# Optimization experiments

Measured on AMD Instinct MI355X. Metric: run time of the kernel, lower is better.

The kernel has to match this reference:

```python
import jax, jax.numpy as jnp
import numpy as np

B, L, D = 8, 8192, 128
NC, N, H = 8, 64, 16          # chunks, d_state, chunk_size
NLAYERS, COND, RED = 3, 32, 64
OUT_DIMS = (1, 1, 100, 192, 64, 12, 5)  # f0,A,amps,hmag,nmag,formants(4*3),expression


def _ln(x, g, b, eps=1e-5):
    m = jnp.mean(x, -1, keepdims=True)
    v = jnp.mean((x - m) ** 2, -1, keepdims=True)
    return (x - m) / jnp.sqrt(v + eps) * g + b


def _s4_block(x, g, b, inW, inb, outW, outb, lre, lim, Bn, Cre, Cim, Dc):
    # ParallelS4Layer: LN -> in_proj -> per-chunk S4 FFT conv (fused/batched) -> out_proj -> SiLU -> residual
    Bt, Lt, Dt = x.shape
    z = _ln(x, g, b) @ inW + inb
    u = z.reshape(Bt, Lt, NC, H)
    t = jnp.arange(Lt, dtype=jnp.float32)
    E = jnp.exp((lre + 1j * lim)[:, :, None] * t)                       # [NC,N,L] Vandermonde
    k = jnp.real(jnp.einsum('cn,cnl->cl', (Cre + 1j * Cim) * Bn, E))    # [NC,L]
    k = jnp.concatenate([k, k[:, ::-1]], axis=-1)                        # bidirectional -> [NC,2L]
    kf = jnp.fft.rfft(k, n=2 * Lt, axis=-1)                              # [NC,L+1]
    uf = jnp.fft.rfft(u, n=2 * Lt, axis=1)                               # [B,L+1,NC,H]
    y = jnp.fft.irfft(uf * kf.T[None, :, :, None], n=2 * Lt, axis=1)[:, :Lt]
    y = (y + u * Dc[None, None, :, None]).reshape(Bt, Lt, Dt)           # skip term D
    return x + jax.nn.silu(y @ outW + outb)


def _forward(f0, phone_emb, singer_emb, lang_emb, inW, inb, inln_g, inln_b,
             s4_ln_g, s4_ln_b, s4_inW, s4_inb, s4_outW, s4_outb,
             lam_re, lam_im, Bn, C_re, C_im, Dc,
             attn_g, attn_lnb, attn_w, attn_bias, gpW, gpb,
             genW_s, genb_s, genW_sh, genb_sh, genW_h, genb_h, genW_o, genb_o,
             phone_seq, singer_id, language_id):
    Bt, Lt = phone_seq.shape
    pe = phone_emb[phone_seq]                                            # [B,L,64]
    se = jnp.broadcast_to(singer_emb[singer_id][:, None, :], (Bt, Lt, singer_emb.shape[1]))
    le = jnp.broadcast_to(lang_emb[language_id][:, None, :], (Bt, Lt, lang_emb.shape[1]))
    x = jnp.concatenate([pe, se, le, f0], axis=-1)                       # [B,L,113]
    h = jax.nn.silu(_ln(x @ inW + inb, inln_g, inln_b))                  # input_proj
    for i in range(NLAYERS):
        h = _s4_block(h, s4_ln_g[i], s4_ln_b[i], s4_inW[i], s4_inb[i],
                      s4_outW[i], s4_outb[i], lam_re[i], lam_im[i],
                      Bn[i], C_re[i], C_im[i], Dc[i])
    logits = _ln(h, attn_g, attn_lnb) @ attn_w + attn_bias[0]            # [B,L]
    a = jax.nn.softmax(logits, axis=1)
    g = jnp.einsum('bl,bld->bd', a, h) @ gpW + gpb                       # global cond [B,32]
    outs = []
    for i, d in enumerate(OUT_DIMS):
        scale = (g @ genW_s[i] + genb_s[i])[:, None, :]
        shift = (g @ genW_sh[i] + genb_sh[i])[:, None, :]
        r = jax.nn.silu((h * scale + shift) @ genW_h[i] + genb_h[i])
        outs.append(r @ genW_o[i, :, :d] + genb_o[i, :d])
    return jnp.concatenate(outs, axis=-1)                                # [B,L,375]


def setup_inputs() -> dict:
    ks = iter(jax.random.split(jax.random.key(0), 64))
    nk = lambda: next(ks)
    w = lambda *s: jax.random.normal(nk(), s, jnp.float32) * 0.02
    CIN = 64 + 32 + 16 + 1
    return {
        'phone_seq': jax.random.randint(nk(), (B, L), 0, 100),
        'singer_id': jax.random.randint(nk(), (B,), 0, 50),
        'language_id': jax.random.randint(nk(), (B,), 0, 10),
        'f0': jax.random.uniform(nk(), (B, L, 1), jnp.float32),
        'phone_emb': w(100, 64), 'singer_emb': w(50, 32), 'lang_emb': w(10, 16),
        'inW': w(CIN, D), 'inb': jnp.zeros((D,), jnp.float32),
        'inln_g': jnp.ones((D,), jnp.float32), 'inln_b': jnp.zeros((D,), jnp.float32),
        's4_ln_g': jnp.ones((NLAYERS, D), jnp.float32), 's4_ln_b': jnp.zeros((NLAYERS, D), jnp.float32),
        's4_inW': w(NLAYERS, D, D), 's4_inb': jnp.zeros((NLAYERS, D), jnp.float32),
        's4_outW': w(NLAYERS, D, D), 's4_outb': jnp.zeros((NLAYERS, D), jnp.float32),
        'lam_re': -0.5 * jnp.ones((NLAYERS, NC, N), jnp.float32),
        'lam_im': jnp.broadcast_to(jnp.arange(N, dtype=jnp.float32) * (2.0 * np.pi / N), (NLAYERS, NC, N)),
        'Bn': jax.random.normal(nk(), (NLAYERS, NC, N), jnp.float32),
        'C_re': jax.random.normal(nk(), (NLAYERS, NC, N), jnp.float32),
        'C_im': jax.random.normal(nk(), (NLAYERS, NC, N), jnp.float32),
        'Dc': jax.random.normal(nk(), (NLAYERS, NC), jnp.float32),
        'attn_g': jnp.ones((D,), jnp.float32), 'attn_lnb': jnp.zeros((D,), jnp.float32),
        'attn_w': w(D), 'attn_bias': jnp.zeros((1,), jnp.float32),
        'gpW': w(D, COND), 'gpb': jnp.zeros((COND,), jnp.float32),
        'genW_s': w(7, COND, D), 'genb_s': jnp.zeros((7, D), jnp.float32),
        'genW_sh': w(7, COND, D), 'genb_sh': jnp.zeros((7, D), jnp.float32),
        'genW_h': w(7, D, RED), 'genb_h': jnp.zeros((7, RED), jnp.float32),
        'genW_o': w(7, RED, 192), 'genb_o': jnp.zeros((7, 192), jnp.float32),
    }


def reference(phone_seq, singer_id, language_id, f0, phone_emb, singer_emb, lang_emb,
              inW, inb, inln_g, inln_b, s4_ln_g, s4_ln_b, s4_inW, s4_inb, s4_outW, s4_outb,
              lam_re, lam_im, Bn, C_re, C_im, Dc, attn_g, attn_lnb, attn_w, attn_bias,
              gpW, gpb, genW_s, genb_s, genW_sh, genb_sh, genW_h, genb_h, genW_o, genb_o):
    return _forward(f0, phone_emb, singer_emb, lang_emb, inW, inb, inln_g, inln_b,
                    s4_ln_g, s4_ln_b, s4_inW, s4_inb, s4_outW, s4_outb,
                    lam_re, lam_im, Bn, C_re, C_im, Dc,
                    attn_g, attn_lnb, attn_w, attn_bias, gpW, gpb,
                    genW_s, genb_s, genW_sh, genb_sh, genW_h, genb_h, genW_o, genb_o,
                    phone_seq, singer_id, language_id)
```

## Files before the change

### kernel.cpp

```cpp
#include <hip/hip_runtime.h>
#include <math.h>

#define BB 8
#define LL 8192
#define DD 128
#define NCH 8
#define NST 64
#define TAPS 32
#define NOUTD 375
#define NSEG 64

typedef __attribute__((ext_vector_type(8))) short bf16x8;
typedef __attribute__((ext_vector_type(4))) float f32x4;
#define MFMA16(a,b,c) __builtin_amdgcn_mfma_f32_16x16x32_bf16((a),(b),(c),0,0,0)

struct __align__(8) us4 { unsigned short x,y,z,w; };

__device__ __forceinline__ unsigned short f2b(float f) {
  unsigned x = __float_as_uint(f);
  unsigned r = (x + 0x7fffu + ((x >> 16) & 1u)) >> 16;
  return (unsigned short)r;
}
__device__ __forceinline__ float b2f(unsigned short u) {
  return __uint_as_float(((unsigned)u) << 16);
}
__device__ __forceinline__ float silu_f(float x){ return x / (1.f + expf(-x)); }

static constexpr size_t WS_H      = 0;
static constexpr size_t WS_LOGITS = WS_H      + (size_t)BB*LL*DD;
static constexpr size_t WS_SEGM   = WS_LOGITS + (size_t)BB*LL;
static constexpr size_t WS_SEGS   = WS_SEGM   + BB*NSEG;
static constexpr size_t WS_SEGV   = WS_SEGS   + BB*NSEG;
static constexpr size_t WS_SCALE  = WS_SEGV   + (size_t)BB*NSEG*DD;
static constexpr size_t WS_SHIFT  = WS_SCALE  + (size_t)7*BB*DD;
static constexpr size_t WS_C1     = WS_SHIFT  + (size_t)7*BB*DD;
static constexpr size_t WS_C2     = WS_C1     + 3*DD;
static constexpr size_t WS_KTAB   = WS_C2     + 3*DD;
static constexpr size_t WS_GAW    = WS_KTAB   + 3*NCH*TAPS;
static constexpr size_t WS_ASCAL  = WS_GAW    + DD;
static constexpr size_t WS_BASE   = WS_ASCAL  + 32;
static constexpr size_t WS_BIAS1  = WS_BASE   + BB*DD;
static constexpr size_t WS_ZB_F   = WS_BIAS1  + (size_t)BB*448;
static constexpr size_t WS_WGT_F  = WS_ZB_F   + (size_t)BB*LL*DD/2;
static constexpr size_t WS_WOT_F  = WS_WGT_F  + (size_t)3*DD*DD/2;
static constexpr size_t WS_WO2T_F = WS_WOT_F  + (size_t)3*DD*DD/2;
static constexpr size_t WS_WCT_F  = WS_WO2T_F + (size_t)7*192*64/2;
static constexpr size_t WS_TOTAL  = WS_WCT_F  + (size_t)BB*448*DD/2;

__device__ __constant__ int c_offs_d[7] = {0, 1, 2, 102, 294, 358, 370};
__device__ __constant__ int c_dims_d[7] = {1, 1, 100, 192, 64, 12, 5};
__device__ __constant__ int t_hd[27] = {0,1,2,2,2,2,2,2,2,3,3,3,3,3,3,3,3,3,3,3,3,4,4,4,4,5,6};
__device__ __constant__ int t_nl[27] = {0,0,0,1,2,3,4,5,6,0,1,2,3,4,5,6,7,8,9,10,11,0,1,2,3,0,0};

__global__ __launch_bounds__(256) void k0_setup(
    const float* s4_ln_g, const float* s4_ln_b, const float* s4_inW, const float* s4_inb,
    const float* s4_outW,
    const float* lam_re, const float* lam_im, const float* Bn, const float* Cre, const float* Cim,
    const float* attn_g, const float* attn_lnb, const float* attn_w, const float* attn_bias,
    const int* singer_id, const int* language_id,
    const float* singer_emb, const float* lang_emb, const float* inW, const float* inb,
    const float* genW_o, float* ws)
{
  int blk = blockIdx.x, tid = threadIdx.x;
  if (blk < 3) {
    __shared__ __align__(16) unsigned short tile[128*136];
    __shared__ float c1p[256], c2p[256];
    int ly = blk;
    int n = tid & 127;
    float c1a = 0.f, c2a = 0.f;
    for (int j = 0; j < 64; ++j) {
      int k = (tid >> 7) + 2*j;
      float v  = s4_inW[((size_t)ly*DD + k)*DD + n];
      float gk = s4_ln_g[ly*DD + k];
      float bk = s4_ln_b[ly*DD + k];
      tile[k*136 + n] = f2b(gk*v);
      c1a += gk*v; c2a += bk*v;
    }
    c1p[tid] = c1a; c2p[tid] = c2a;
    __syncthreads();
    if (tid < DD) {
      ws[WS_C1 + ly*DD + tid] = c1p[tid] + c1p[tid+128];
      ws[WS_C2 + ly*DD + tid] = c2p[tid] + c2p[tid+128] + s4_inb[ly*DD + tid];
    }
    unsigned short* wgt = (unsigned short*)(ws + WS_WGT_F);
    for (int o = tid; o < DD*DD; o += 256) {
      int nn = o >> 7, k = o & 127;
      wgt[ly*DD*DD + o] = tile[k*136 + nn];
    }
    __syncthreads();
    for (int j = 0; j < 64; ++j) {
      int k = (tid >> 7) + 2*j;
      tile[k*136 + n] = f2b(s4_outW[((size_t)ly*DD + k)*DD + n]);
    }
    __syncthreads();
    unsigned short* wot = (unsigned short*)(ws + WS_WOT_F);
    for (int o = tid; o < DD*DD; o += 256) {
      int nn = o >> 7, k = o & 127;
      wot[ly*DD*DD + o] = tile[k*136 + nn];
    }
  } else if (blk < 27) {
    __shared__ float part[256];
    int ly = (blk - 3) >> 3, cx = (blk - 3) & 7;
    int dt = tid & 31, nc = tid >> 5;
    const float* lre = lam_re + (ly*NCH + cx)*NST;
    const float* lim = lam_im + (ly*NCH + cx)*NST;
    const float* bn  = Bn  + (ly*NCH + cx)*NST;
    const float* cre = Cre + (ly*NCH + cx)*NST;
    const float* cim = Cim + (ly*NCH + cx)*NST;
    float td = (float)dt, acc = 0.f;
    for (int nn = nc*8; nn < nc*8 + 8; ++nn) {
      float e = expf(lre[nn]*td);
      float ang = lim[nn]*td;
      acc += bn[nn]*(cre[nn]*cosf(ang) - cim[nn]*sinf(ang))*e;
    }
    part[tid] = acc;
    __syncthreads();
    if (tid < 32) {
      float a = 0.f;
      #pragma unroll
      for (int i = 0; i < 8; ++i) a += part[i*32 + tid];
      ws[WS_KTAB + (ly*NCH + cx)*TAPS + tid] = a;
    }
  } else if (blk == 27) {
    for (int o = tid; o < BB*DD; o += 256) {
      int b = o >> 7, d = o & 127;
      int sid = singer_id[b], lid = language_id[b];
      float acc = inb[d];
      for (int j = 0; j < 32; ++j) acc += singer_emb[sid*32 + j]*inW[(64 + j)*DD + d];
      for (int j = 0; j < 16; ++j) acc += lang_emb[lid*16 + j]*inW[(96 + j)*DD + d];
      ws[WS_BASE + o] = acc;
    }
    if (tid < DD) ws[WS_GAW + tid] = attn_g[tid]*attn_w[tid];
    if (tid == 0) {
      float c1s = 0.f, c2s = 0.f;
      for (int d = 0; d < DD; ++d) { c1s += attn_g[d]*attn_w[d]; c2s += attn_lnb[d]*attn_w[d]; }
      ws[WS_ASCAL+0] = c1s;
      ws[WS_ASCAL+1] = c2s + attn_bias[0];
    }
  } else {
    __shared__ float gw[64*200];
    int hd = blk - 28;
    for (int k = 0; k < 64; ++k) {
      if (tid < 192) gw[k*200 + tid] = genW_o[((size_t)hd*64 + k)*192 + tid];
    }
    __syncthreads();
    unsigned short* wo2t = (unsigned short*)(ws + WS_WO2T_F);
    for (int o = tid; o < 192*64; o += 256) {
      int nn = o >> 6, k = o & 63;
      wo2t[(size_t)hd*192*64 + o] = f2b(gw[k*200 + nn]);
    }
  }
}

__global__ __launch_bounds__(256) void k1p_input(
    const int* phone_seq, const float* f0, const float* phone_emb,
    const float* inW, const float* inln_g, const float* inln_b, float* ws)
{
  __shared__ __align__(16) float pm[64*72];
  __shared__ __align__(16) unsigned short hm[64*136];
  __shared__ int   ps[64];
  __shared__ float fv[64];
  __shared__ float rs_s[64], mrs_s[64];
  int tid = threadIdx.x;
  size_t gbase = (size_t)blockIdx.x * 64;
  if (tid < 64) { ps[tid] = phone_seq[gbase + tid]; fv[tid] = f0[gbase + tid]; }
  __syncthreads();
  #pragma unroll
  for (int j = 0; j < 4; ++j) {
    int idx4 = tid + 256*j;
    int tok = idx4 >> 4, col = idx4 & 15;
    float4 v = *(const float4*)(phone_emb + (size_t)ps[tok]*64 + col*4);
    *(float4*)(pm + tok*72 + col*4) = v;
  }
  __syncthreads();
  int ti = tid >> 5, di = tid & 31, d0 = di*4;
  float acc[8][4];
  #pragma unroll
  for (int i = 0; i < 8; ++i) { acc[i][0]=0.f; acc[i][1]=0.f; acc[i][2]=0.f; acc[i][3]=0.f; }
  for (int kk = 0; kk < 64; kk += 4) {
    float4 w0 = *(const float4*)(inW + (kk+0)*DD + d0);
    float4 w1 = *(const float4*)(inW + (kk+1)*DD + d0);
    float4 w2 = *(const float4*)(inW + (kk+2)*DD + d0);
    float4 w3 = *(const float4*)(inW + (kk+3)*DD + d0);
    #pragma unroll
    for (int i = 0; i < 8; ++i) {
      float4 a = *(float4*)(pm + (ti*8 + i)*72 + kk);
      acc[i][0] += a.x*w0.x + a.y*w1.x + a.z*w2.x + a.w*w3.x;
      acc[i][1] += a.x*w0.y + a.y*w1.y + a.z*w2.y + a.w*w3.y;
      acc[i][2] += a.x*w0.z + a.y*w1.z + a.z*w2.z + a.w*w3.z;
      acc[i][3] += a.x*w0.w + a.y*w1.w + a.z*w2.w + a.w*w3.w;
    }
  }
  float4 w112 = *(const float4*)(inW + 112*DD + d0);
  int b = (int)(gbase >> 13);
  float4 bs  = *(const float4*)(ws + WS_BASE + b*DD + d0);
  float4 lg4 = *(const float4*)(inln_g + d0);
  float4 lb4 = *(const float4*)(inln_b + d0);
  float s2[8], ss2[8];
  #pragma unroll
  for (int i = 0; i < 8; ++i) {
    int tok = ti*8 + i;
    float fz = fv[tok];
    float y0 = acc[i][0] + fz*w112.x + bs.x;
    float y1 = acc[i][1] + fz*w112.y + bs.y;
    float y2 = acc[i][2] + fz*w112.z + bs.z;
    float y3 = acc[i][3] + fz*w112.w + bs.w;
    float s  = y0+y1+y2+y3;
    float ss = y0*y0+y1*y1+y2*y2+y3*y3;
    #pragma unroll
    for (int m = 16; m >= 1; m >>= 1) { s += __shfl_xor(s, m); ss += __shfl_xor(ss, m); }
    float mean = s * 0.0078125f;
    float var  = ss * 0.0078125f - mean*mean;
    float rstd = rsqrtf(var + 1e-5f);
    y0 = silu_f((y0 - mean)*rstd*lg4.x + lb4.x);
    y1 = silu_f((y1 - mean)*rstd*lg4.y + lb4.y);
    y2 = silu_f((y2 - mean)*rstd*lg4.z + lb4.z);
    y3 = silu_f((y3 - mean)*rstd*lg4.w + lb4.w);
    *(float4*)(ws + WS_H + (gbase + tok)*DD + d0) = make_float4(y0,y1,y2,y3);
    us4 p; p.x = f2b(y0); p.y = f2b(y1); p.z = f2b(y2); p.w = f2b(y3);
    *(us4*)(hm + tok*136 + d0) = p;
    s2[i]  = y0+y1+y2+y3;
    ss2[i] = y0*y0+y1*y1+y2*y2+y3*y3;
  }
  #pragma unroll
  for (int m = 16; m >= 1; m >>= 1) {
    #pragma unroll
    for (int i = 0; i < 8; ++i) { s2[i] += __shfl_xor(s2[i], m); ss2[i] += __shfl_xor(ss2[i], m); }
  }
  if (di == 0) {
    #pragma unroll
    for (int i = 0; i < 8; ++i) {
      int tok = ti*8 + i;
      float mean = s2[i]*0.0078125f;
      float var  = ss2[i]*0.0078125f - mean*mean;
      float rstd = rsqrtf(var + 1e-5f);
      rs_s[tok] = rstd; mrs_s[tok] = mean*rstd;
    }
  }
  __syncthreads();
  int w = tid >> 6, lane = tid & 63, q = lane >> 4, c = lane & 15;
  int m16 = w*16;
  const unsigned short* wgt = (const unsigned short*)(ws + WS_WGT_F);
  bf16x8 aF[4];
  #pragma unroll
  for (int kk = 0; kk < 4; ++kk)
    aF[kk] = *(const bf16x8*)(hm + (m16 + c)*136 + kk*32 + q*8);
  float rsv[4], mrv[4];
  #pragma unroll
  for (int r = 0; r < 4; ++r) { int row = m16 + q*4 + r; rsv[r] = rs_s[row]; mrv[r] = mrs_s[row]; }
  unsigned short* zb = (unsigned short*)(ws + WS_ZB_F);
  #pragma unroll
  for (int nt = 0; nt < 8; ++nt) {
    f32x4 za = {0.f,0.f,0.f,0.f};
    #pragma unroll
    for (int kk = 0; kk < 4; ++kk) {
      bf16x8 bF = *(const bf16x8*)(wgt + (nt*16 + c)*DD + kk*32 + q*8);
      za = MFMA16(aF[kk], bF, za);
    }
    int col = nt*16 + c;
    float c1v = ws[WS_C1 + col];
    float c2v = ws[WS_C2 + col];
    #pragma unroll
    for (int r = 0; r < 4; ++r) {
      float zv = rsv[r]*za[r] - mrv[r]*c1v + c2v;
      zb[(gbase + m16 + q*4 + r)*DD + col] = f2b(zv);
    }
  }
}

__global__ __launch_bounds__(256) void k3p_conv_out(
    float* ws, const float* s4_outb, const float* Dc, int ly, int do_logits, int do_z)
{
  __shared__ __align__(16) unsigned short zw[128*128];
  __shared__ __align__(16) unsigned short ym[64*136];
  __shared__ float k2t[8*64];
  __shared__ float dcs[8];
  __shared__ float rs2[64], mrs2[64];
  int tid = threadIdx.x, blk = blockIdx.x;
  int b  = blk >> 7;
  int t0 = (blk & 127) * 64;
  const unsigned short* zbp = (const unsigned short*)(ws + WS_ZB_F);
  #pragma unroll
  for (int j = 0; j < 8; ++j) {
    int idx8 = tid + 256*j;
    int tok = idx8 >> 4, c8 = idx8 & 15;
    int t = t0 - 32 + tok;
    bf16x8 v = {0,0,0,0,0,0,0,0};
    if (t >= 0 && t < LL) v = *(const bf16x8*)(zbp + ((size_t)b*LL + t)*DD + c8*8);
    *(bf16x8*)(zw + tok*DD + c8*8) = v;
  }
  for (int o = tid; o < 512; o += 256) {
    int c = o >> 6, m = o & 63;
    int idx = (m <= 31) ? (31 - m) : (m - 32);
    k2t[o] = ws[WS_KTAB + (ly*NCH + c)*TAPS + idx];
  }
  if (tid < 8) dcs[tid] = Dc[ly*NCH + tid];
  __syncthreads();
  #pragma unroll
  for (int p = 0; p < 2; ++p) {
    int half = p*2 + (tid >> 7), ch = tid & 127, cx = ch >> 4;
    int base = 1 + half*16;
    float ring[16], accv[16];
    #pragma unroll
    for (int x = 0; x < 16; ++x) { ring[x] = b2f(zw[(base + x)*DD + ch]); accv[x] = 0.f; }
    #pragma unroll
    for (int m = 0; m < 64; ++m) {
      float kf = k2t[cx*64 + m];
      #pragma unroll
      for (int i = 0; i < 16; ++i) accv[i] += kf * ring[(m + i) & 15];
      if (m < 63) ring[m & 15] = b2f(zw[(base + m + 16)*DD + ch]);
    }
    float dcv = dcs[cx];
    #pragma unroll
    for (int i = 0; i < 16; ++i) {
      int tl = half*16 + i;
      ym[tl*136 + ch] = f2b(accv[i] + dcv * b2f(zw[(32 + tl)*DD + ch]));
    }
  }
  __syncthreads();
  unsigned short* hm2 = zw;
  int w = tid >> 6, lane = tid & 63, q = lane >> 4, c = lane & 15;
  int m16 = w*16;
  const unsigned short* wot = (const unsigned short*)(ws + WS_WOT_F) + ly*DD*DD;
  bf16x8 aF[4];
  #pragma unroll
  for (int kk = 0; kk < 4; ++kk)
    aF[kk] = *(const bf16x8*)(ym + (m16 + c)*136 + kk*32 + q*8);
  float* hbuf = ws + WS_H;
  float c1s = ws[WS_ASCAL+0], c2s = ws[WS_ASCAL+1];
  float sr[4] = {0,0,0,0}, ssr[4] = {0,0,0,0}, dtr[4] = {0,0,0,0};
  #pragma unroll
  for (int nt = 0; nt < 8; ++nt) {
    f32x4 acc = {0.f,0.f,0.f,0.f};
    #pragma unroll
    for (int kk = 0; kk < 4; ++kk) {
      bf16x8 bF = *(const bf16x8*)(wot + (nt*16 + c)*DD + kk*32 + q*8);
      acc = MFMA16(aF[kk], bF, acc);
    }
    int col = nt*16 + c;
    float ob = s4_outb[ly*DD + col];
    float gw = ws[WS_GAW + col];
    #pragma unroll
    for (int r = 0; r < 4; ++r) {
      size_t gofs = ((size_t)b*LL + t0 + m16 + q*4 + r)*DD + col;
      float hold = hbuf[gofs];
      float hn = hold + silu_f(acc[r] + ob);
      hbuf[gofs] = hn;
      hm2[(m16 + q*4 + r)*136 + col] = f2b(hn);
      sr[r] += hn; ssr[r] += hn*hn;
      if (do_logits) dtr[r] += hn*gw;
    }
  }
  #pragma unroll
  for (int m = 8; m >= 1; m >>= 1) {
    #pragma unroll
    for (int r = 0; r < 4; ++r) {
      sr[r]  += __shfl_xor(sr[r],  m);
      ssr[r] += __shfl_xor(ssr[r], m);
      if (do_logits) dtr[r] += __shfl_xor(dtr[r], m);
    }
  }
  if (c < 4) {
    int r = c;
    float mean = sr[r]*0.0078125f;
    float var  = ssr[r]*0.0078125f - mean*mean;
    float rstd = rsqrtf(var + 1e-5f);
    int row = m16 + q*4 + r;
    if (do_z) { rs2[row] = rstd; mrs2[row] = mean*rstd; }
    if (do_logits)
      ws[WS_LOGITS + (size_t)b*LL + t0 + row] = rstd*dtr[r] - mean*rstd*c1s + c2s;
  }
  if (do_z) {
    __syncthreads();
    const unsigned short* wgt2 = (const unsigned short*)(ws + WS_WGT_F) + (ly+1)*DD*DD;
    bf16x8 aF2[4];
    #pragma unroll
    for (int kk = 0; kk < 4; ++kk)
      aF2[kk] = *(const bf16x8*)(hm2 + (m16 + c)*136 + kk*32 + q*8);
    float rsv[4], mrv[4];
    #pragma unroll
    for (int r = 0; r < 4; ++r) { int row = m16 + q*4 + r; rsv[r] = rs2[row]; mrv[r] = mrs2[row]; }
    unsigned short* zb = (unsigned short*)(ws + WS_ZB_F);
    size_t gbase = (size_t)b*LL + t0;
    #pragma unroll
    for (int nt = 0; nt < 8; ++nt) {
      f32x4 za = {0.f,0.f,0.f,0.f};
      #pragma unroll
      for (int kk = 0; kk < 4; ++kk) {
        bf16x8 bF = *(const bf16x8*)(wgt2 + (nt*16 + c)*DD + kk*32 + q*8);
        za = MFMA16(aF2[kk], bF, za);
      }
      int col = nt*16 + c;
      float c1v = ws[WS_C1 + (ly+1)*DD + col];
      float c2v = ws[WS_C2 + (ly+1)*DD + col];
      #pragma unroll
      for (int r = 0; r < 4; ++r) {
        float zv = rsv[r]*za[r] - mrv[r]*c1v + c2v;
        zb[(gbase + m16 + q*4 + r)*DD + col] = f2b(zv);
      }
    }
  }
}

__global__ __launch_bounds__(256) void k5b_pool(float* ws)
{
  int blk = blockIdx.x, tid = threadIdx.x;
  int b = blk >> 6, seg = blk & 63;
  const float* lg = ws + WS_LOGITS + (size_t)b*LL + seg*128;
  __shared__ float ev[128];
  __shared__ float red[4], red2[4];
  __shared__ float vr[2][128];
  float a0 = (tid < 128) ? lg[tid] : -1e30f;
  float mx = a0;
  #pragma unroll
  for (int m = 32; m >= 1; m >>= 1) mx = fmaxf(mx, __shfl_xor(mx, m));
  if ((tid & 63) == 0) red[tid >> 6] = mx;
  __syncthreads();
  float M = fmaxf(fmaxf(red[0], red[1]), fmaxf(red[2], red[3]));
  float e0 = (tid < 128) ? expf(a0 - M) : 0.f;
  if (tid < 128) ev[tid] = e0;
  float s = e0;
  #pragma unroll
  for (int m = 32; m >= 1; m >>= 1) s += __shfl_xor(s, m);
  if ((tid & 63) == 0) red2[tid >> 6] = s;
  __syncthreads();
  float S = red2[0] + red2[1] + red2[2] + red2[3];
  int ls = tid >> 7, d = tid & 127;
  const float* hb = ws + WS_H + ((size_t)b*LL + seg*128)*DD;
  float acc = 0.f;
  for (int jj = 0; jj < 64; ++jj) {
    int tok = jj*2 + ls;
    acc += ev[tok] * hb[(size_t)tok*DD + d];
  }
  vr[ls][d] = acc;
  __syncthreads();
  if (tid < 128) ws[WS_SEGV + (size_t)(b*NSEG + seg)*DD + tid] = vr[0][tid] + vr[1][tid];
  if (tid == 0) { ws[WS_SEGM + b*NSEG + seg] = M; ws[WS_SEGS + b*NSEG + seg] = S; }
}

__global__ __launch_bounds__(256) void k5c_cond(
    float* ws, const float* gpW, const float* gpb,
    const float* genW_s, const float* genb_s, const float* genW_sh, const float* genb_sh)
{
  __shared__ float wsg[NSEG];
  __shared__ float Ssh[1];
  __shared__ float gpre[DD];
  __shared__ float red[256];
  __shared__ float gg[32];
  int b = blockIdx.x, tid = threadIdx.x;
  if (tid == 0) {
    float M = -1e30f;
    for (int sg = 0; sg < NSEG; ++sg) M = fmaxf(M, ws[WS_SEGM + b*NSEG + sg]);
    float S = 0.f;
    for (int sg = 0; sg < NSEG; ++sg) {
      float e = expf(ws[WS_SEGM + b*NSEG + sg] - M);
      wsg[sg] = e;
      S += ws[WS_SEGS + b*NSEG + sg]*e;
    }
    Ssh[0] = S;
  }
  __syncthreads();
  if (tid < DD) {
    float V = 0.f;
    for (int sg = 0; sg < NSEG; ++sg)
      V += ws[WS_SEGV + (size_t)(b*NSEG + sg)*DD + tid]*wsg[sg];
    gpre[tid] = V / Ssh[0];
  }
  __syncthreads();
  {
    int c = tid & 31, kc = tid >> 5;
    float p = 0.f;
    for (int k = kc*16; k < kc*16 + 16; ++k) p += gpre[k]*gpW[k*32 + c];
    red[tid] = p;
  }
  __syncthreads();
  if (tid < 32) {
    float a = gpb[tid];
    #pragma unroll
    for (int i = 0; i < 8; ++i) a += red[i*32 + tid];
    gg[tid] = a;
  }
  __syncthreads();
  for (int o = tid; o < 7*DD; o += 256) {
    int hd = o >> 7, d = o & 127;
    float sc = genb_s[hd*DD + d], sh = genb_sh[hd*DD + d];
    for (int c = 0; c < 32; ++c) {
      float g = gg[c];
      sc += g*genW_s[((size_t)hd*32 + c)*DD + d];
      sh += g*genW_sh[((size_t)hd*32 + c)*DD + d];
    }
    ws[WS_SCALE + (size_t)hd*BB*DD + b*DD + d] = sc;
    ws[WS_SHIFT + (size_t)hd*BB*DD + b*DD + d] = sh;
  }
}

__global__ __launch_bounds__(256) void k5d_fold(float* ws, const float* genW_h, const float* genb_h)
{
  __shared__ float wh[128*65];
  __shared__ float red[256];
  int hd = blockIdx.x, tid = threadIdx.x;
  for (int o = tid; o < DD*64; o += 256) {
    int k = o >> 6, j = o & 63;
    wh[k*65 + j] = genW_h[(size_t)hd*DD*64 + o];
  }
  __syncthreads();
  unsigned short* wct = (unsigned short*)(ws + WS_WCT_F);
  for (int b = 0; b < BB; ++b) {
    const float* sc = ws + WS_SCALE + (size_t)hd*BB*DD + b*DD;
    const float* sh = ws + WS_SHIFT + (size_t)hd*BB*DD + b*DD;
    for (int o = tid; o < 64*DD; o += 256) {
      int j = o >> 7, k = o & 127;
      wct[((size_t)b*448 + hd*64 + j)*DD + k] = f2b(sc[k]*wh[k*65 + j]);
    }
    {
      int j = tid >> 2, kc = tid & 3;
      float p = 0.f;
      for (int k = kc*32; k < kc*32 + 32; ++k) p += sh[k]*wh[k*65 + j];
      red[tid] = p;
      __syncthreads();
      if (tid < 64)
        ws[WS_BIAS1 + b*448 + hd*64 + tid] =
          genb_h[hd*64 + tid] + red[tid*4] + red[tid*4+1] + red[tid*4+2] + red[tid*4+3];
      __syncthreads();
    }
  }
}

__global__ __launch_bounds__(512) void k6_heads(float* ws, const float* genb_o, float* out, int blk0)
{
  __shared__ __align__(16) unsigned short hm[64*136];
  __shared__ __align__(16) unsigned short rm[64*456];
  int tid = threadIdx.x, blk = blockIdx.x + blk0;
  int b = blk >> 7, t0 = (blk & 127)*64;
  const float* hb = ws + WS_H + ((size_t)b*LL + t0)*DD;
  #pragma unroll
  for (int j = 0; j < 4; ++j) {
    int idx4 = tid + 512*j;
    int tok = idx4 >> 5, c4 = idx4 & 31;
    float4 v = *(const float4*)(hb + (size_t)idx4*4);
    us4 p; p.x = f2b(v.x); p.y = f2b(v.y); p.z = f2b(v.z); p.w = f2b(v.w);
    *(us4*)(hm + tok*136 + c4*4) = p;
  }
  __syncthreads();
  int w = tid >> 6, lane = tid & 63, q = lane >> 4, c = lane & 15;
  int mi = w & 3, nh = w >> 2;
  int m16 = mi*16;
  {
    bf16x8 aF[4];
    #pragma unroll
    for (int kk = 0; kk < 4; ++kk)
      aF[kk] = *(const bf16x8*)(hm + (m16 + c)*136 + kk*32 + q*8);
    const unsigned short* wct = (const unsigned short*)(ws + WS_WCT_F) + (size_t)b*448*DD;
    #pragma unroll 2
    for (int ntl = 0; ntl < 14; ++ntl) {
      int nt = nh*14 + ntl;
      f32x4 acc = {0.f,0.f,0.f,0.f};
      #pragma unroll
      for (int kk = 0; kk < 4; ++kk) {
        bf16x8 bF = *(const bf16x8*)(wct + ((size_t)nt*16 + c)*DD + kk*32 + q*8);
        acc = MFMA16(aF[kk], bF, acc);
      }
      int col = nt*16 + c;
      float bias = ws[WS_BIAS1 + b*448 + col];
      #pragma unroll
      for (int r = 0; r < 4; ++r)
        rm[(m16 + q*4 + r)*456 + col] = f2b(silu_f(acc[r] + bias));
    }
  }
  __syncthreads();
  {
    const unsigned short* wo2t = (const unsigned short*)(ws + WS_WO2T_F);
    int i0 = (nh == 0) ? 0 : 14;
    int i1 = (nh == 0) ? 14 : 27;
    #pragma unroll 2
    for (int i = i0; i < i1; ++i) {
      int hd = t_hd[i], nl = t_nl[i];
      bf16x8 aF0 = *(const bf16x8*)(rm + (m16 + c)*456 + hd*64 + q*8);
      bf16x8 aF1 = *(const bf16x8*)(rm + (m16 + c)*456 + hd*64 + 32 + q*8);
      f32x4 acc = {0.f,0.f,0.f,0.f};
      bf16x8 bF0 = *(const bf16x8*)(wo2t + ((size_t)hd*192 + nl*16 + c)*64 + q*8);
      bf16x8 bF1 = *(const bf16x8*)(wo2t + ((size_t)hd*192 + nl*16 + c)*64 + 32 + q*8);
      acc = MFMA16(aF0, bF0, acc);
      acc = MFMA16(aF1, bF1, acc);
      int cl = nl*16 + c;
      int di = c_dims_d[hd];
      if (cl < di) {
        float bo = genb_o[hd*192 + cl];
        #pragma unroll
        for (int r = 0; r < 4; ++r)
          out[((size_t)b*LL + t0 + m16 + q*4 + r)*NOUTD + c_offs_d[hd] + cl] = acc[r] + bo;
      }
    }
  }
}

extern "C" void kernel_launch(void* const* d_in, const int* in_sizes, int n_in,
                              void* d_out, int out_size, void* d_ws, size_t ws_size,
                              hipStream_t stream) {
  const int*   phone_seq   = (const int*)  d_in[0];
  const int*   singer_id   = (const int*)  d_in[1];
  const int*   language_id = (const int*)  d_in[2];
  const float* f0          = (const float*)d_in[3];
  const float* phone_emb   = (const float*)d_in[4];
  const float* singer_emb  = (const float*)d_in[5];
  const float* lang_emb    = (const float*)d_in[6];
  const float* inW         = (const float*)d_in[7];
  const float* inb         = (const float*)d_in[8];
  const float* inln_g      = (const float*)d_in[9];
  const float* inln_b      = (const float*)d_in[10];
  const float* s4_ln_g     = (const float*)d_in[11];
  const float* s4_ln_b     = (const float*)d_in[12];
  const float* s4_inW      = (const float*)d_in[13];
  const float* s4_inb      = (const float*)d_in[14];
  const float* s4_outW     = (const float*)d_in[15];
  const float* s4_outb     = (const float*)d_in[16];
  const float* lam_re      = (const float*)d_in[17];
  const float* lam_im      = (const float*)d_in[18];
  const float* Bn          = (const float*)d_in[19];
  const float* C_re        = (const float*)d_in[20];
  const float* C_im        = (const float*)d_in[21];
  const float* Dc          = (const float*)d_in[22];
  const float* attn_g      = (const float*)d_in[23];
  const float* attn_lnb    = (const float*)d_in[24];
  const float* attn_w      = (const float*)d_in[25];
  const float* attn_bias   = (const float*)d_in[26];
  const float* gpW         = (const float*)d_in[27];
  const float* gpb         = (const float*)d_in[28];
  const float* genW_s      = (const float*)d_in[29];
  const float* genb_s      = (const float*)d_in[30];
  const float* genW_sh     = (const float*)d_in[31];
  const float* genb_sh     = (const float*)d_in[32];
  const float* genW_h      = (const float*)d_in[33];
  const float* genb_h      = (const float*)d_in[34];
  const float* genW_o      = (const float*)d_in[35];
  const float* genb_o      = (const float*)d_in[36];
  float* ws  = (float*)d_ws;
  float* out = (float*)d_out;

  k0_setup<<<35, 256, 0, stream>>>(s4_ln_g, s4_ln_b, s4_inW, s4_inb, s4_outW,
                                   lam_re, lam_im, Bn, C_re, C_im,
                                   attn_g, attn_lnb, attn_w, attn_bias,
                                   singer_id, language_id, singer_emb, lang_emb, inW, inb,
                                   genW_o, ws);
  k1p_input<<<BB*LL/64, 256, 0, stream>>>(phone_seq, f0, phone_emb, inW, inln_g, inln_b, ws);
  for (int ly = 0; ly < 3; ++ly) {
    k3p_conv_out<<<BB*LL/64, 256, 0, stream>>>(ws, s4_outb, Dc, ly,
                                               (ly == 2) ? 1 : 0, (ly < 2) ? 1 : 0);
  }
  k5b_pool<<<BB*NSEG, 256, 0, stream>>>(ws);
  k5c_cond<<<BB, 256, 0, stream>>>(ws, gpW, gpb, genW_s, genb_s, genW_sh, genb_sh);
  k5d_fold<<<7, 256, 0, stream>>>(ws, genW_h, genb_h);
  k6_heads<<<512, 512, 0, stream>>>(ws, genb_o, out, 0);
  k6_heads<<<512, 512, 0, stream>>>(ws, genb_o, out, 512);
}
```

Measured before the change: 618.4 us.

## Parallelize small conditioning kernels and move scale/shift compute into fold kernel

The setup block now stages the embedding weights and the attention vectors in shared memory. The conditioning kernel loads segment values and gpW into LDS and replaces the serial thread-0 softmax reduction with a wave-shuffle reduction. It now writes only the 32-dim conditioning vector. The scale/shift projection, previously done by 8 blocks with strided global reads, moves into the 7-block fold kernel using LDS-staged weights, so the fold reads scale/shift from shared memory instead of global. This targets the latency of the tiny serial tail kernels; the cost is higher LDS use per block.

```diff
diff --git a/kernel.cpp b/kernel.cpp
--- a/kernel.cpp
+++ b/kernel.cpp
@@ -122,18 +122,35 @@
       ws[WS_KTAB + (ly*NCH + cx)*TAPS + tid] = a;
     }
   } else if (blk == 27) {
+    __shared__ float emb[BB*48];
+    __shared__ float w2[48*DD];
+    __shared__ float r1[DD], r2[DD];
+    for (int o = tid; o < 48*DD; o += 256) w2[o] = inW[64*DD + o];
+    if (tid < BB*32) {
+      int b = tid >> 5, j = tid & 31;
+      emb[b*48 + j] = singer_emb[singer_id[b]*32 + j];
+    }
+    if (tid < BB*16) {
+      int b = tid >> 4, j = tid & 15;
+      emb[b*48 + 32 + j] = lang_emb[language_id[b]*16 + j];
+    }
+    if (tid < DD) {
+      float gw_ = attn_g[tid]*attn_w[tid];
+      float bw  = attn_lnb[tid]*attn_w[tid];
+      ws[WS_GAW + tid] = gw_;
+      r1[tid] = gw_; r2[tid] = bw;
+    }
+    __syncthreads();
     for (int o = tid; o < BB*DD; o += 256) {
       int b = o >> 7, d = o & 127;
-      int sid = singer_id[b], lid = language_id[b];
       float acc = inb[d];
-      for (int j = 0; j < 32; ++j) acc += singer_emb[sid*32 + j]*inW[(64 + j)*DD + d];
-      for (int j = 0; j < 16; ++j) acc += lang_emb[lid*16 + j]*inW[(96 + j)*DD + d];
+      #pragma unroll
+      for (int j = 0; j < 48; ++j) acc += emb[b*48 + j]*w2[j*DD + d];
       ws[WS_BASE + o] = acc;
     }
-    if (tid < DD) ws[WS_GAW + tid] = attn_g[tid]*attn_w[tid];
     if (tid == 0) {
       float c1s = 0.f, c2s = 0.f;
-      for (int d = 0; d < DD; ++d) { c1s += attn_g[d]*attn_w[d]; c2s += attn_lnb[d]*attn_w[d]; }
+      for (int d = 0; d < DD; ++d) { c1s += r1[d]; c2s += r2[d]; }
       ws[WS_ASCAL+0] = c1s;
       ws[WS_ASCAL+1] = c2s + attn_bias[0];
     }
@@ -439,38 +456,55 @@
 }
 
 __global__ __launch_bounds__(256) void k5c_cond(
-    float* ws, const float* gpW, const float* gpb,
-    const float* genW_s, const float* genb_s, const float* genW_sh, const float* genb_sh)
+    float* ws, const float* gpW, const float* gpb)
 {
+  __shared__ float segv[NSEG*DD];
+  __shared__ float gpwl[DD*32];
   __shared__ float wsg[NSEG];
-  __shared__ float Ssh[1];
+  __shared__ float Ssh;
   __shared__ float gpre[DD];
+  __shared__ float vr[2][DD];
   __shared__ float red[256];
-  __shared__ float gg[32];
   int b = blockIdx.x, tid = threadIdx.x;
-  if (tid == 0) {
-    float M = -1e30f;
-    for (int sg = 0; sg < NSEG; ++sg) M = fmaxf(M, ws[WS_SEGM + b*NSEG + sg]);
-    float S = 0.f;
-    for (int sg = 0; sg < NSEG; ++sg) {
-      float e = expf(ws[WS_SEGM + b*NSEG + sg] - M);
-      wsg[sg] = e;
-      S += ws[WS_SEGS + b*NSEG + sg]*e;
-    }
-    Ssh[0] = S;
-  }
-  __syncthreads();
-  if (tid < DD) {
+  #pragma unroll
+  for (int j = 0; j < 8; ++j) {
+    int i4 = tid + 256*j;
+    *(float4*)(segv + i4*4) = *(const float4*)(ws + WS_SEGV + (size_t)b*NSEG*DD + i4*4);
+  }
+  #pragma unroll
+  for (int j = 0; j < 4; ++j) {
+    int i4 = tid + 256*j;
+    *(float4*)(gpwl + i4*4) = *(const float4*)(gpW + i4*4);
+  }
+  if (tid < 64) {
+    float m = ws[WS_SEGM + b*NSEG + tid];
+    float s = ws[WS_SEGS + b*NSEG + tid];
+    float M = m;
+    #pragma unroll
+    for (int x = 32; x >= 1; x >>= 1) M = fmaxf(M, __shfl_xor(M, x));
+    float e = expf(m - M);
+    float Sp = s*e;
+    #pragma unroll
+    for (int x = 32; x >= 1; x >>= 1) Sp += __shfl_xor(Sp, x);
+    wsg[tid] = e;
+    if (tid == 0) Ssh = Sp;
+  }
+  __syncthreads();
+  {
+    int ls = tid >> 7, d = tid & 127;
     float V = 0.f;
-    for (int sg = 0; sg < NSEG; ++sg)
-      V += ws[WS_SEGV + (size_t)(b*NSEG + sg)*DD + tid]*wsg[sg];
-    gpre[tid] = V / Ssh[0];
-  }
+    #pragma unroll
+    for (int sg = ls*32; sg < ls*32 + 32; ++sg)
+      V += segv[sg*DD + d]*wsg[sg];
+    vr[ls][d] = V;
+  }
+  __syncthreads();
+  if (tid < DD) gpre[tid] = (vr[0][tid] + vr[1][tid]) / Ssh;
   __syncthreads();
   {
     int c = tid & 31, kc = tid >> 5;
     float p = 0.f;
-    for (int k = kc*16; k < kc*16 + 16; ++k) p += gpre[k]*gpW[k*32 + c];
+    for (int k = kc*16; k < kc*16 + 16; ++k) p += gpre[k]*gpwl[k*32 + c];
     red[tid] = p;
   }
   __syncthreads();
@@ -478,44 +512,56 @@
     float a = gpb[tid];
     #pragma unroll
     for (int i = 0; i < 8; ++i) a += red[i*32 + tid];
-    gg[tid] = a;
-  }
-  __syncthreads();
-  for (int o = tid; o < 7*DD; o += 256) {
-    int hd = o >> 7, d = o & 127;
-    float sc = genb_s[hd*DD + d], sh = genb_sh[hd*DD + d];
-    for (int c = 0; c < 32; ++c) {
-      float g = gg[c];
-      sc += g*genW_s[((size_t)hd*32 + c)*DD + d];
-      sh += g*genW_sh[((size_t)hd*32 + c)*DD + d];
-    }
-    ws[WS_SCALE + (size_t)hd*BB*DD + b*DD + d] = sc;
-    ws[WS_SHIFT + (size_t)hd*BB*DD + b*DD + d] = sh;
-  }
-}
-
-__global__ __launch_bounds__(256) void k5d_fold(float* ws, const float* genW_h, const float* genb_h)
+    ws[WS_SCALE + b*32 + tid] = a;
+  }
+}
+
+__global__ __launch_bounds__(256) void k5d_fold(
+    float* ws, const float* genW_h, const float* genb_h,
+    const float* genW_s, const float* genb_s, const float* genW_sh, const float* genb_sh)
 {
   __shared__ float wh[128*65];
+  __shared__ float gsw[32*DD];
+  __shared__ float ghw[32*DD];
+  __shared__ float ggs[BB*32];
+  __shared__ float scs[BB*DD];
+  __shared__ float shs[BB*DD];
   __shared__ float red[256];
   int hd = blockIdx.x, tid = threadIdx.x;
   for (int o = tid; o < DD*64; o += 256) {
     int k = o >> 6, j = o & 63;
     wh[k*65 + j] = genW_h[(size_t)hd*DD*64 + o];
   }
+  #pragma unroll
+  for (int j = 0; j < 4; ++j) {
+    int i4 = tid + 256*j;
+    *(float4*)(gsw + i4*4) = *(const float4*)(genW_s  + (size_t)hd*32*DD + i4*4);
+    *(float4*)(ghw + i4*4) = *(const float4*)(genW_sh + (size_t)hd*32*DD + i4*4);
+  }
+  ggs[tid] = ws[WS_SCALE + tid];
+  __syncthreads();
+  for (int o = tid; o < BB*DD; o += 256) {
+    int b = o >> 7, d = o & 127;
+    float sc = genb_s[hd*DD + d], sh = genb_sh[hd*DD + d];
+    #pragma unroll
+    for (int c = 0; c < 32; ++c) {
+      float g = ggs[b*32 + c];
+      sc += g*gsw[c*DD + d];
+      sh += g*ghw[c*DD + d];
+    }
+    scs[o] = sc; shs[o] = sh;
+  }
   __syncthreads();
   unsigned short* wct = (unsigned short*)(ws + WS_WCT_F);
   for (int b = 0; b < BB; ++b) {
-    const float* sc = ws + WS_SCALE + (size_t)hd*BB*DD + b*DD;
-    const float* sh = ws + WS_SHIFT + (size_t)hd*BB*DD + b*DD;
     for (int o = tid; o < 64*DD; o += 256) {
       int j = o >> 7, k = o & 127;
-      wct[((size_t)b*448 + hd*64 + j)*DD + k] = f2b(sc[k]*wh[k*65 + j]);
+      wct[((size_t)b*448 + hd*64 + j)*DD + k] = f2b(scs[b*DD + k]*wh[k*65 + j]);
     }
     {
       int j = tid >> 2, kc = tid & 3;
       float p = 0.f;
-      for (int k = kc*32; k < kc*32 + 32; ++k) p += sh[k]*wh[k*65 + j];
+      for (int k = kc*32; k < kc*32 + 32; ++k) p += shs[b*DD + k]*wh[k*65 + j];
       red[tid] = p;
       __syncthreads();
       if (tid < 64)
@@ -648,8 +694,8 @@
                                                (ly == 2) ? 1 : 0, (ly < 2) ? 1 : 0);
   }
   k5b_pool<<<BB*NSEG, 256, 0, stream>>>(ws);
-  k5c_cond<<<BB, 256, 0, stream>>>(ws, gpW, gpb, genW_s, genb_s, genW_sh, genb_sh);
-  k5d_fold<<<7, 256, 0, stream>>>(ws, genW_h, genb_h);
+  k5c_cond<<<BB, 256, 0, stream>>>(ws, gpW, gpb);
+  k5d_fold<<<7, 256, 0, stream>>>(ws, genW_h, genb_h, genW_s, genb_s, genW_sh, genb_sh);
   k6_heads<<<512, 512, 0, stream>>>(ws, genb_o, out, 0);
   k6_heads<<<512, 512, 0, stream>>>(ws, genb_o, out, 512);
 }
```

Result: faster. 514.3 us (-16.8%).
